# Kernel optimization log

Hardware: AMD Instinct MI355X
Metric: run time of the kernel (lower is better)

Reference implementation:

```python
import jax, jax.numpy as jnp
import numpy as np

R = 8                 # level-0 resolution (voxels per block side)
STRIDE = 8**3 + 2**3  # 520: total voxels per block across levels [8,2]
OFFSET = 0            # level-0 offset into the per-block voxel buffer
V = 0.01              # level-0 voxel size
G = 32                # dense block-grid side (stand-in for sparse hashmap domain)
CAP = 20000           # hashmap capacity (allocated blocks)
N = 2_000_000         # query points
F = 5                 # feature dim: 1 sdf + 1 weight + 3 rgb

_CORNERS = jnp.array([[i, j, k] for i in (0, 1) for j in (0, 1) for k in (0, 1)], dtype=jnp.int32)  # [8,3]


def setup_inputs() -> dict:
    key = jax.random.key(0)
    k1, k2, k3 = jax.random.split(key, 3)
    block_size = V * R
    # query points inside the active domain [0, G*block_size)
    x = jax.random.uniform(k1, (N, 3), dtype=jnp.float32) * (G * block_size)
    feat_params = jax.random.normal(k2, (CAP, STRIDE, F), dtype=jnp.float32) * 0.1
    # hashmap stand-in: unique block indices for CAP of the G^3 block coords, -1 = empty
    perm = jax.random.permutation(k3, G ** 3)
    block_table = jnp.where(perm < CAP, perm, -1).reshape(G, G, G).astype(jnp.int32)
    return {"x": x, "feat_params": feat_params, "block_table": block_table}


def reference(x, feat_params, block_table):
    # sparse multi-res voxel feature gather + trilinear interp + analytic grad (level 0)
    u = x / V                                  # global voxel-space coords
    xi = jnp.floor(u).astype(jnp.int32)        # [N,3] base voxel
    frac = u - xi                              # [N,3] trilinear fractions
    gv = xi[:, None, :] + _CORNERS[None]       # [N,8,3] corner voxel coords
    bc = jnp.floor_divide(gv, R)               # block coords per corner
    lc = gv - bc * R                           # in-block voxel coords
    inb = jnp.all((bc >= 0) & (bc < G), axis=-1)           # [N,8]
    bcs = jnp.clip(bc, 0, G - 1)
    bidx = block_table[bcs[..., 0], bcs[..., 1], bcs[..., 2]]  # [N,8] hashmap lookup
    found = inb & (bidx >= 0)
    masks = jnp.all(found, axis=1)             # [N] all 8 corners allocated
    bsafe = jnp.maximum(bidx, 0)
    vidx = OFFSET + (lc[..., 0] * R + lc[..., 1]) * R + lc[..., 2]  # [N,8]
    f = feat_params[bsafe, vidx]               # [N,8,F] irregular gather
    # trilinear weights and their spatial derivatives
    w01 = jnp.stack([1.0 - frac, frac], axis=-1)                        # [N,3,2]
    P = w01[:, jnp.arange(3)[None, :], _CORNERS]                        # [N,8,3]
    S = (2 * _CORNERS - 1).astype(x.dtype)                              # [8,3] d(w)/d(u)
    w = P[..., 0] * P[..., 1] * P[..., 2]                               # [N,8]
    dw = jnp.stack([S[None, :, 0] * P[..., 1] * P[..., 2],
                    P[..., 0] * S[None, :, 1] * P[..., 2],
                    P[..., 0] * P[..., 1] * S[None, :, 2]], axis=-1)    # [N,8,3]
    m = masks.astype(x.dtype)
    feats = jnp.einsum('nc,ncf->nf', w, f) * m[:, None]                 # [N,F]
    dfeats_dx = jnp.einsum('ncd,ncf->nfd', dw, f) * (m[:, None, None] / V)  # [N,F,3]
    return feats, dfeats_dx, masks
```

## Files before the change

### kernel.cpp

```cpp
#include <hip/hip_runtime.h>
#include <math.h>

#define NPTS 2000000
#define GG 32
#define FF 5
#define BLK 256

typedef float v4f __attribute__((ext_vector_type(4)));

__global__ __launch_bounds__(256) void hashgrid_kernel(
    const float* __restrict__ x,
    const float* __restrict__ feat,
    const int* __restrict__ btab,
    float* __restrict__ out)
{
    __shared__ float smem[5120];
    const int tid  = threadIdx.x;
    const int bid  = blockIdx.x;
    const int base = bid * BLK;
    const int cnt  = min(BLK, NPTS - base);

    {
        const float4* xin = (const float4*)(x + (size_t)base * 3);
        float4* s4 = (float4*)smem;
        int nf4 = (cnt * 3) >> 2;
        for (int i = tid; i < nf4; i += BLK) s4[i] = xin[i];
    }
    __syncthreads();

    float x0 = 0.f, x1 = 0.f, x2 = 0.f;
    if (tid < cnt) { x0 = smem[tid*3+0]; x1 = smem[tid*3+1]; x2 = smem[tid*3+2]; }
    __syncthreads();

    float accf[5] = {0,0,0,0,0};
    float adx[5]  = {0,0,0,0,0};
    float ady[5]  = {0,0,0,0,0};
    float adz[5]  = {0,0,0,0,0};
    float mval = 0.f;

    if (tid < cnt) {
        float u0 = x0 * 100.0f, u1 = x1 * 100.0f, u2 = x2 * 100.0f;
        float fl0 = floorf(u0), fl1 = floorf(u1), fl2 = floorf(u2);
        int xi0 = (int)fl0, xi1 = (int)fl1, xi2 = (int)fl2;
        float fr0 = u0 - fl0, fr1 = u1 - fl1, fr2 = u2 - fl2;

        int vidx[8]; bool inb[8]; int bv[8];
        #pragma unroll
        for (int c = 0; c < 8; ++c) {
            int i = (c >> 2) & 1, j = (c >> 1) & 1, k = c & 1;
            int g0 = xi0 + i, g1 = xi1 + j, g2 = xi2 + k;
            int b0 = g0 >> 3, b1 = g1 >> 3, b2 = g2 >> 3;
            inb[c] = ((unsigned)b0 < GG) & ((unsigned)b1 < GG) & ((unsigned)b2 < GG);
            int c0 = min(max(b0,0),GG-1), c1 = min(max(b1,0),GG-1), c2 = min(max(b2,0),GG-1);
            vidx[c] = ((g0 & 7) * 8 + (g1 & 7)) * 8 + (g2 & 7);
            const int* bp = btab + ((c0 * GG + c1) * GG + c2);
            asm volatile("global_load_dword %0, %1, off"
                         : "=v"(bv[c]) : "v"(bp));
        }
        asm volatile("s_waitcnt vmcnt(0)"
                     : "+v"(bv[0]), "+v"(bv[1]), "+v"(bv[2]), "+v"(bv[3]),
                       "+v"(bv[4]), "+v"(bv[5]), "+v"(bv[6]), "+v"(bv[7]));
        __builtin_amdgcn_sched_barrier(0);

        bool ok = true;
        int offs[8];
        #pragma unroll
        for (int c = 0; c < 8; ++c) {
            ok &= inb[c] & (bv[c] >= 0);
            offs[c] = max(bv[c], 0) * 520 + vidx[c];
        }

        if (ok) {
            mval = 1.f;
            float p0[2] = {1.f - fr0, fr0};
            float p1[2] = {1.f - fr1, fr1};
            float p2[2] = {1.f - fr2, fr2};

            v4f q[8]; float t[8];
            #pragma unroll
            for (int c = 0; c < 8; ++c) {
                const float* fp = feat + (size_t)offs[c] * 5;
                asm volatile("global_load_dwordx4 %0, %1, off"
                             : "=v"(q[c]) : "v"(fp));
                asm volatile("global_load_dword %0, %1, off offset:16"
                             : "=v"(t[c]) : "v"(fp));
            }
            asm volatile("s_waitcnt vmcnt(0)"
                         : "+v"(q[0]), "+v"(q[1]), "+v"(q[2]), "+v"(q[3]),
                           "+v"(q[4]), "+v"(q[5]), "+v"(q[6]), "+v"(q[7]),
                           "+v"(t[0]), "+v"(t[1]), "+v"(t[2]), "+v"(t[3]),
                           "+v"(t[4]), "+v"(t[5]), "+v"(t[6]), "+v"(t[7]));
            __builtin_amdgcn_sched_barrier(0);

            #pragma unroll
            for (int c = 0; c < 8; ++c) {
                int i = (c >> 2) & 1, j = (c >> 1) & 1, k = c & 1;
                float wi = p0[i], wj = p1[j], wk = p2[k];
                float si = i ? 1.f : -1.f;
                float sj = j ? 1.f : -1.f;
                float sk = k ? 1.f : -1.f;
                float w   = wi * wj * wk;
                float dwx = si * wj * wk;
                float dwy = wi * sj * wk;
                float dwz = wi * wj * sk;
                float vv[5] = {q[c][0], q[c][1], q[c][2], q[c][3], t[c]};
                #pragma unroll
                for (int f = 0; f < 5; ++f) {
                    float v = vv[f];
                    accf[f] += w   * v;
                    adx[f]  += dwx * v;
                    ady[f]  += dwy * v;
                    adz[f]  += dwz * v;
                }
            }
        }
    }

    if (tid < cnt) {
        float* fs = smem + tid * 5;
        #pragma unroll
        for (int f = 0; f < 5; ++f) fs[f] = accf[f];
        float* ds = smem + 1280 + tid * 15;
        #pragma unroll
        for (int f = 0; f < 5; ++f) {
            ds[f*3+0] = adx[f] * 100.0f;
            ds[f*3+1] = ady[f] * 100.0f;
            ds[f*3+2] = adz[f] * 100.0f;
        }
        out[(size_t)NPTS * 20 + base + tid] = mval;
    }
    __syncthreads();

    {
        const float4* s4 = (const float4*)smem;
        float4* o = (float4*)(out + (size_t)base * 5);
        int nf4 = (cnt * 5) >> 2;
        for (int i = tid; i < nf4; i += BLK) o[i] = s4[i];
    }
    {
        const float4* s4 = (const float4*)(smem + 1280);
        float4* o = (float4*)(out + (size_t)NPTS * 5 + (size_t)base * 15);
        int nf4 = (cnt * 15) >> 2;
        for (int i = tid; i < nf4; i += BLK) o[i] = s4[i];
    }
}

extern "C" void kernel_launch(void* const* d_in, const int* in_sizes, int n_in,
                              void* d_out, int out_size, void* d_ws, size_t ws_size,
                              hipStream_t stream) {
    const float* x    = (const float*)d_in[0];
    const float* feat = (const float*)d_in[1];
    const int*   btab = (const int*)d_in[2];
    float* out = (float*)d_out;
    int blocks = (NPTS + BLK - 1) / BLK;
    hashgrid_kernel<<<blocks, BLK, 0, stream>>>(x, feat, btab, out);
}
```

Baseline: 436.1 us.

## Fast path: single block lookup and paired z-corner feature loads

When the query's base voxel does not sit at the last index of its block along any axis, all 8 corners fall in one block, so the kernel issues a single hashmap lookup instead of eight. When the z-corners do not cross a block boundary, the two z-adjacent corners are contiguous in memory (10 floats), so each pair is fetched with dwordx4+dwordx4+dwordx2 loads rather than two x4+x1 pairs. This cuts the number of dependent global loads and memory instructions per point. The cost is branch divergence between the fast and fallback paths within a wavefront, plus a larger code footprint.

Result: faster. 410.3 us (-5.9%).

```diff
diff --git a/kernel.cpp b/kernel.cpp
--- a/kernel.cpp
+++ b/kernel.cpp
@@ -7,6 +7,7 @@
 #define BLK 256
 
 typedef float v4f __attribute__((ext_vector_type(4)));
+typedef float v2f __attribute__((ext_vector_type(2)));
 
 __global__ __launch_bounds__(256) void hashgrid_kernel(
     const float* __restrict__ x,
@@ -44,30 +45,51 @@
         int xi0 = (int)fl0, xi1 = (int)fl1, xi2 = (int)fl2;
         float fr0 = u0 - fl0, fr1 = u1 - fl1, fr2 = u2 - fl2;
 
-        int vidx[8]; bool inb[8]; int bv[8];
+        int vidx[8];
         #pragma unroll
         for (int c = 0; c < 8; ++c) {
             int i = (c >> 2) & 1, j = (c >> 1) & 1, k = c & 1;
-            int g0 = xi0 + i, g1 = xi1 + j, g2 = xi2 + k;
-            int b0 = g0 >> 3, b1 = g1 >> 3, b2 = g2 >> 3;
-            inb[c] = ((unsigned)b0 < GG) & ((unsigned)b1 < GG) & ((unsigned)b2 < GG);
-            int c0 = min(max(b0,0),GG-1), c1 = min(max(b1,0),GG-1), c2 = min(max(b2,0),GG-1);
-            vidx[c] = ((g0 & 7) * 8 + (g1 & 7)) * 8 + (g2 & 7);
-            const int* bp = btab + ((c0 * GG + c1) * GG + c2);
-            asm volatile("global_load_dword %0, %1, off"
-                         : "=v"(bv[c]) : "v"(bp));
-        }
-        asm volatile("s_waitcnt vmcnt(0)"
-                     : "+v"(bv[0]), "+v"(bv[1]), "+v"(bv[2]), "+v"(bv[3]),
-                       "+v"(bv[4]), "+v"(bv[5]), "+v"(bv[6]), "+v"(bv[7]));
-        __builtin_amdgcn_sched_barrier(0);
-
-        bool ok = true;
+            vidx[c] = (((xi0 + i) & 7) * 8 + ((xi1 + j) & 7)) * 8 + ((xi2 + k) & 7);
+        }
+
+        const bool cz = (xi2 & 7) == 7;
+        const bool anycross = ((xi0 & 7) == 7) | ((xi1 & 7) == 7) | cz;
+
         int offs[8];
-        #pragma unroll
-        for (int c = 0; c < 8; ++c) {
-            ok &= inb[c] & (bv[c] >= 0);
-            offs[c] = max(bv[c], 0) * 520 + vidx[c];
+        bool ok;
+        if (!anycross) {
+            const int* bp = btab + (((xi0 >> 3) * GG + (xi1 >> 3)) * GG + (xi2 >> 3));
+            int bv;
+            asm volatile("global_load_dword %0, %1, off" : "=&v"(bv) : "v"(bp));
+            asm volatile("s_waitcnt vmcnt(0)" : "+v"(bv));
+            __builtin_amdgcn_sched_barrier(0);
+            ok = bv >= 0;
+            int bo = max(bv, 0) * 520;
+            #pragma unroll
+            for (int c = 0; c < 8; ++c) offs[c] = bo + vidx[c];
+        } else {
+            bool inb[8]; int bv[8];
+            #pragma unroll
+            for (int c = 0; c < 8; ++c) {
+                int i = (c >> 2) & 1, j = (c >> 1) & 1, k = c & 1;
+                int g0 = xi0 + i, g1 = xi1 + j, g2 = xi2 + k;
+                int b0 = g0 >> 3, b1 = g1 >> 3, b2 = g2 >> 3;
+                inb[c] = ((unsigned)b0 < GG) & ((unsigned)b1 < GG) & ((unsigned)b2 < GG);
+                int c0 = min(max(b0,0),GG-1), c1 = min(max(b1,0),GG-1), c2 = min(max(b2,0),GG-1);
+                const int* bp = btab + ((c0 * GG + c1) * GG + c2);
+                asm volatile("global_load_dword %0, %1, off"
+                             : "=&v"(bv[c]) : "v"(bp));
+            }
+            asm volatile("s_waitcnt vmcnt(0)"
+                         : "+v"(bv[0]), "+v"(bv[1]), "+v"(bv[2]), "+v"(bv[3]),
+                           "+v"(bv[4]), "+v"(bv[5]), "+v"(bv[6]), "+v"(bv[7]));
+            __builtin_amdgcn_sched_barrier(0);
+            ok = true;
+            #pragma unroll
+            for (int c = 0; c < 8; ++c) {
+                ok &= inb[c] & (bv[c] >= 0);
+                offs[c] = max(bv[c], 0) * 520 + vidx[c];
+            }
         }
 
         if (ok) {
@@ -76,41 +98,97 @@
             float p1[2] = {1.f - fr1, fr1};
             float p2[2] = {1.f - fr2, fr2};
 
-            v4f q[8]; float t[8];
-            #pragma unroll
-            for (int c = 0; c < 8; ++c) {
-                const float* fp = feat + (size_t)offs[c] * 5;
-                asm volatile("global_load_dwordx4 %0, %1, off"
-                             : "=v"(q[c]) : "v"(fp));
-                asm volatile("global_load_dword %0, %1, off offset:16"
-                             : "=v"(t[c]) : "v"(fp));
-            }
-            asm volatile("s_waitcnt vmcnt(0)"
-                         : "+v"(q[0]), "+v"(q[1]), "+v"(q[2]), "+v"(q[3]),
-                           "+v"(q[4]), "+v"(q[5]), "+v"(q[6]), "+v"(q[7]),
-                           "+v"(t[0]), "+v"(t[1]), "+v"(t[2]), "+v"(t[3]),
-                           "+v"(t[4]), "+v"(t[5]), "+v"(t[6]), "+v"(t[7]));
-            __builtin_amdgcn_sched_barrier(0);
-
-            #pragma unroll
-            for (int c = 0; c < 8; ++c) {
-                int i = (c >> 2) & 1, j = (c >> 1) & 1, k = c & 1;
-                float wi = p0[i], wj = p1[j], wk = p2[k];
-                float si = i ? 1.f : -1.f;
-                float sj = j ? 1.f : -1.f;
-                float sk = k ? 1.f : -1.f;
-                float w   = wi * wj * wk;
-                float dwx = si * wj * wk;
-                float dwy = wi * sj * wk;
-                float dwz = wi * wj * sk;
-                float vv[5] = {q[c][0], q[c][1], q[c][2], q[c][3], t[c]};
-                #pragma unroll
-                for (int f = 0; f < 5; ++f) {
-                    float v = vv[f];
-                    accf[f] += w   * v;
-                    adx[f]  += dwx * v;
-                    ady[f]  += dwy * v;
-                    adz[f]  += dwz * v;
+            if (!cz) {
+                v4f A[4], B[4]; v2f C[4];
+                #pragma unroll
+                for (int p = 0; p < 4; ++p) {
+                    const float* fp = feat + (size_t)offs[p*2] * 5;
+                    asm volatile("global_load_dwordx4 %0, %1, off"
+                                 : "=&v"(A[p]) : "v"(fp));
+                    asm volatile("global_load_dwordx4 %0, %1, off offset:16"
+                                 : "=&v"(B[p]) : "v"(fp));
+                    asm volatile("global_load_dwordx2 %0, %1, off offset:32"
+                                 : "=&v"(C[p]) : "v"(fp));
+                }
+                asm volatile("s_waitcnt vmcnt(0)"
+                             : "+v"(A[0]), "+v"(A[1]), "+v"(A[2]), "+v"(A[3]),
+                               "+v"(B[0]), "+v"(B[1]), "+v"(B[2]), "+v"(B[3]),
+                               "+v"(C[0]), "+v"(C[1]), "+v"(C[2]), "+v"(C[3]));
+                __builtin_amdgcn_sched_barrier(0);
+
+                #pragma unroll
+                for (int p = 0; p < 4; ++p) {
+                    int i = (p >> 1) & 1, j = p & 1;
+                    float wi = p0[i], wj = p1[j];
+                    float si = i ? 1.f : -1.f;
+                    float sj = j ? 1.f : -1.f;
+                    float wij = wi * wj;
+                    float dxy = si * wj;
+                    float dyx = wi * sj;
+                    {
+                        float wk = p2[0];
+                        float w = wij * wk, dwx = dxy * wk, dwy = dyx * wk, dwz = -wij;
+                        float vv[5] = {A[p][0], A[p][1], A[p][2], A[p][3], B[p][0]};
+                        #pragma unroll
+                        for (int f = 0; f < 5; ++f) {
+                            float v = vv[f];
+                            accf[f] += w   * v;
+                            adx[f]  += dwx * v;
+                            ady[f]  += dwy * v;
+                            adz[f]  += dwz * v;
+                        }
+                    }
+                    {
+                        float wk = p2[1];
+                        float w = wij * wk, dwx = dxy * wk, dwy = dyx * wk, dwz = wij;
+                        float vv[5] = {B[p][1], B[p][2], B[p][3], C[p][0], C[p][1]};
+                        #pragma unroll
+                        for (int f = 0; f < 5; ++f) {
+                            float v = vv[f];
+                            accf[f] += w   * v;
+                            adx[f]  += dwx * v;
+                            ady[f]  += dwy * v;
+                            adz[f]  += dwz * v;
+                        }
+                    }
+                }
+            } else {
+                v4f q[8]; float t[8];
+                #pragma unroll
+                for (int c = 0; c < 8; ++c) {
+                    const float* fp = feat + (size_t)offs[c] * 5;
+                    asm volatile("global_load_dwordx4 %0, %1, off"
+                                 : "=&v"(q[c]) : "v"(fp));
+                    asm volatile("global_load_dword %0, %1, off offset:16"
+                                 : "=&v"(t[c]) : "v"(fp));
+                }
+                asm volatile("s_waitcnt vmcnt(0)"
+                             : "+v"(q[0]), "+v"(q[1]), "+v"(q[2]), "+v"(q[3]),
+                               "+v"(q[4]), "+v"(q[5]), "+v"(q[6]), "+v"(q[7]),
+                               "+v"(t[0]), "+v"(t[1]), "+v"(t[2]), "+v"(t[3]),
+                               "+v"(t[4]), "+v"(t[5]), "+v"(t[6]), "+v"(t[7]));
+                __builtin_amdgcn_sched_barrier(0);
+
+                #pragma unroll
+                for (int c = 0; c < 8; ++c) {
+                    int i = (c >> 2) & 1, j = (c >> 1) & 1, k = c & 1;
+                    float wi = p0[i], wj = p1[j], wk = p2[k];
+                    float si = i ? 1.f : -1.f;
+                    float sj = j ? 1.f : -1.f;
+                    float sk = k ? 1.f : -1.f;
+                    float w   = wi * wj * wk;
+                    float dwx = si * wj * wk;
+                    float dwy = wi * sj * wk;
+                    float dwz = wi * wj * sk;
+                    float vv[5] = {q[c][0], q[c][1], q[c][2], q[c][3], t[c]};
+                    #pragma unroll
+                    for (int f = 0; f < 5; ++f) {
+                        float v = vv[f];
+                        accf[f] += w   * v;
+                        adx[f]  += dwx * v;
+                        ady[f]  += dwy * v;
+                        adz[f]  += dwz * v;
+                    }
                 }
             }
         }
```
